# Kernel tuning notes

Measured on AMD Instinct MI355X. Metric: run time of the kernel, lower is better.

## Reference

```python
import jax, jax.numpy as jnp
import numpy as np

B, D, O = 16384, 1024, 2048
MU, LAM = 0.9, 0.1


def setup_inputs() -> dict:
    key = jax.random.key(0)
    ks = jax.random.split(key, 16)
    stdv = float(1.0 / np.sqrt(D))
    u = lambda k, shape, s: jax.random.uniform(k, shape, jnp.float32, -s, s)
    return {
        "x": jax.random.normal(ks[0], (B, D), jnp.float32),
        "x_ctx": jax.random.normal(ks[1], (B, D), jnp.float32),
        "classifier": u(ks[2], (O, D), stdv),
        "none_tensor": u(ks[3], (1, D), stdv),
        "ctx_q_w": u(ks[4], (O, D), stdv),
        "ctx_q_b": u(ks[5], (O,), stdv),
        "word_g_w": u(ks[6], (1, D), stdv),
        "word_g_b": u(ks[7], (1,), stdv),
        "tcq_w1": u(ks[8], (D, D), stdv),
        "tcq_b1": u(ks[9], (D,), stdv),
        "tcq_w2": u(ks[10], (O, D), stdv),
        "tcq_b2": u(ks[11], (O,), stdv),
        "history_input": 0.1 * jax.random.normal(ks[12], (O - 1, D), jnp.float32),
        "history_count": jax.random.randint(ks[13], (O - 1,), 0, 10),
        "labels": jax.random.randint(ks[14], (B,), 0, O),
    }


def reference(x, x_ctx, classifier, none_tensor, ctx_q_w, ctx_q_b,
              word_g_w, word_g_b, tcq_w1, tcq_b1, tcq_w2, tcq_b2,
              history_input, history_count, labels):
    mu, lam = MU, LAM
    # ---- update_history (torch.no_grad), vectorized over classes via segment_sum ----
    xs = jax.lax.stop_gradient(x)
    sums = jax.ops.segment_sum(xs, labels, num_segments=O)               # [O, D]
    counts = jax.ops.segment_sum(jnp.ones((B,), jnp.float32), labels, num_segments=O)  # [O]
    has = counts[1:] > 0                                                  # classes 1..O-1
    cls_mean = sums[1:] / jnp.maximum(counts[1:], 1.0)[:, None]
    hist = jnp.where(has[:, None], mu * history_input + cls_mean, history_input)
    cnt = history_count + has.astype(history_count.dtype)
    # ---- generate_substitute (mu < 1 branch) ----
    denom = 1.0 - jnp.power(mu, jnp.maximum(cnt, 1).astype(jnp.float32))[:, None]
    v = hist * (1.0 - mu) / denom                                        # [O-1, D]
    r_sub = jnp.concatenate([none_tensor, v], axis=0)                    # [O, D]
    ctx_logits = x_ctx @ ctx_q_w.T + ctx_q_b                              # [B, O]
    att_logits = jax.nn.gelu(x @ tcq_w1.T + tcq_b1, approximate=False) @ tcq_w2.T + tcq_b2  # [B, O]
    # ---- gated combine + bilinear classifier (training=True path: w uses ctx_logits) ----
    g_word = jax.nn.sigmoid(x @ word_g_w.T + word_g_b)                    # [B, 1]
    w = g_word * jax.nn.sigmoid(ctx_logits)                               # [B, O]
    # logits = sum(((1-w)*x[:,None,:] + w*r_sub) * classifier, -1), collapsed algebraically
    logits = (1.0 - w) * (x @ classifier.T) + w * jnp.einsum('od,od->o', r_sub, classifier)[None, :]
    # ---- losses on labels >= 0 (mask-weighted means, jit-safe) ----
    mask = (labels >= 0).astype(jnp.float32)
    n = jnp.maximum(mask.sum(), 1.0)
    lsm = jax.nn.log_softmax(logits, axis=-1)
    nll = -jnp.take_along_axis(lsm, jnp.maximum(labels, 0)[:, None], axis=1)[:, 0]
    ce = (mask * nll).sum() / n
    mse_row = jnp.mean((ctx_logits - att_logits) ** 2, axis=-1)
    mse = (mask * mse_row).sum() / n
    return (ce + lam * mse, logits)
```

## Files before the change

kernel.cpp:

```cpp
#include <hip/hip_runtime.h>
#include <cstdint>
#include <cstddef>

#define DEV __device__ __forceinline__

typedef __attribute__((ext_vector_type(4))) float f32x4;
typedef __attribute__((ext_vector_type(8))) short bf16x8;
typedef unsigned short ushort_t;
typedef __attribute__((ext_vector_type(8))) unsigned short ushort8;

static constexpr int B_ = 16384, D_ = 1024, O_ = 2048;
static constexpr float LAM_ = 0.1f;

static constexpr size_t WS_XBF   = 0;
static constexpr size_t WS_XCBF  = WS_XBF   + (size_t)B_ * D_ * 2;
static constexpr size_t WS_HBF   = WS_XCBF  + (size_t)B_ * D_ * 2;
static constexpr size_t WS_CLSBF = WS_HBF   + (size_t)B_ * D_ * 2;
static constexpr size_t WS_CTWBF = WS_CLSBF + (size_t)O_ * D_ * 2;
static constexpr size_t WS_W2BF  = WS_CTWBF + (size_t)O_ * D_ * 2;
static constexpr size_t WS_W1BF  = WS_W2BF  + (size_t)O_ * D_ * 2;
static constexpr size_t WS_SMALL = WS_W1BF  + (size_t)D_ * D_ * 2;
static constexpr size_t SM_COUNTS = 0;
static constexpr size_t SM_TSUM   = 8192;
static constexpr size_t SM_MSE    = 16384;
static constexpr size_t SM_ZERO_BYTES = 82176;
static constexpr size_t SM_S      = 82176;
static constexpr size_t SM_GWORD  = 90368;
static constexpr size_t SM_CEROW  = 155904;
static constexpr size_t SM_PMAX   = 262144;
static constexpr size_t SM_PSUM   = 262144 + 524288;
static constexpr size_t WS_CTXBF  = WS_SMALL + 2 * 1024 * 1024;
static constexpr size_t WS_NEED_BIG = WS_CTXBF + (size_t)B_ * O_ * 2;

DEV float wave_sum(float v) {
  #pragma unroll
  for (int o = 32; o; o >>= 1) v += __shfl_xor(v, o, 64);
  return v;
}

DEV ushort_t f2bf1(float f) {
  union { float f; unsigned u; } c{f};
  unsigned r = c.u + 0x7fffu + ((c.u >> 16) & 1u);
  return (ushort_t)(r >> 16);
}

DEV float bf2f(ushort_t u) {
  union { unsigned u; float f; } c{(unsigned)u << 16};
  return c.f;
}

DEV float sigmoidf(float z) { return 1.0f / (1.0f + expf(-z)); }

DEV void gload_lds16(const ushort_t* g, ushort_t* l) {
  __builtin_amdgcn_global_load_lds((const __attribute__((address_space(1))) void*)g,
                                   (__attribute__((address_space(3))) void*)l, 16, 0, 0);
}

DEV void stage2(const ushort_t* __restrict__ s0, ushort_t* slot, int tid) {
  gload_lds16(s0, slot + tid * 8);
  gload_lds16(s0 + 128 * 1024, slot + (tid + 512) * 8);
}

DEV void stage128s(const ushort_t* __restrict__ src, ushort_t* lds_, int tid) {
  int c0 = tid, c1 = tid + 256;
  int q0 = (c0 & 3) ^ ((c0 >> 3) & 3);
  int q1 = (c1 & 3) ^ ((c1 >> 3) & 3);
  gload_lds16(src + (size_t)(c0 >> 2) * 1024 + q0 * 8, lds_ + c0 * 8);
  gload_lds16(src + (size_t)(c1 >> 2) * 1024 + q1 * 8, lds_ + c1 * 8);
}

DEV f32x4 mfma16(bf16x8 a, bf16x8 b, f32x4 c) {
  return __builtin_amdgcn_mfma_f32_16x16x32_bf16(a, b, c, 0, 0, 0);
}

template<int N> DEV void wait_vm() {
  if constexpr (N == 8)      asm volatile("s_waitcnt vmcnt(8)" ::: "memory");
  else if constexpr (N == 4) asm volatile("s_waitcnt vmcnt(4)" ::: "memory");
  else if constexpr (N == 0) asm volatile("s_waitcnt vmcnt(0)" ::: "memory");
}

__global__ __launch_bounds__(256) void f2bf_kernel(const float* __restrict__ in,
                                                   ushort_t* __restrict__ out, int n8) {
  int i = blockIdx.x * 256 + threadIdx.x;
  if (i >= n8) return;
  const float4* p = (const float4*)(in + (size_t)i * 8);
  float4 a = p[0], b = p[1];
  ushort8 o;
  o[0] = f2bf1(a.x); o[1] = f2bf1(a.y); o[2] = f2bf1(a.z); o[3] = f2bf1(a.w);
  o[4] = f2bf1(b.x); o[5] = f2bf1(b.y); o[6] = f2bf1(b.z); o[7] = f2bf1(b.w);
  *(ushort8*)(out + (size_t)i * 8) = o;
}

__global__ __launch_bounds__(256) void rowdot_kernel(const float* __restrict__ x,
    const float* __restrict__ cls, const float* __restrict__ wg,
    const float* __restrict__ wgb, const int* __restrict__ labels,
    float* __restrict__ tsum, float* __restrict__ counts, float* __restrict__ g_word) {
  int wave = threadIdx.x >> 6, lane = threadIdx.x & 63;
  int row = blockIdx.x * 4 + wave;
  const float* xr = x + (size_t)row * D_;
  int lab = labels[row];
  const float* cr = cls + (size_t)max(lab, 0) * D_;
  float t = 0.f, g = 0.f;
  #pragma unroll
  for (int j = 0; j < 4; ++j) {
    int d = j * 256 + lane * 4;
    float4 xv = *(const float4*)(xr + d);
    float4 cv = *(const float4*)(cr + d);
    float4 wv = *(const float4*)(wg + d);
    t += xv.x * cv.x + xv.y * cv.y + xv.z * cv.z + xv.w * cv.w;
    g += xv.x * wv.x + xv.y * wv.y + xv.z * wv.z + xv.w * wv.w;
  }
  t = wave_sum(t); g = wave_sum(g);
  if (lane == 0) {
    if (lab >= 0) {
      atomicAdd(&tsum[lab], t);
      atomicAdd(&counts[lab], 1.0f);
    }
    g_word[row] = sigmoidf(g + wgb[0]);
  }
}

__global__ __launch_bounds__(256) void scls_kernel(const float* __restrict__ cls,
    const float* __restrict__ none_t, const float* __restrict__ hist,
    const int* __restrict__ hcnt, const float* __restrict__ counts,
    const float* __restrict__ tsum, float* __restrict__ s) {
  int wave = threadIdx.x >> 6, lane = threadIdx.x & 63;
  int o = blockIdx.x * 4 + wave;
  if (o >= O_) return;
  const float* cr = cls + (size_t)o * D_;
  const float* src = (o == 0) ? none_t : hist + (size_t)(o - 1) * D_;
  float dv = 0.f;
  #pragma unroll
  for (int j = 0; j < 4; ++j) {
    int d = j * 256 + lane * 4;
    float4 a = *(const float4*)(src + d);
    float4 c = *(const float4*)(cr + d);
    dv += a.x * c.x + a.y * c.y + a.z * c.z + a.w * c.w;
  }
  dv = wave_sum(dv);
  if (lane == 0) {
    if (o == 0) { s[0] = dv; }
    else {
      float co = counts[o];
      bool has = co > 0.f;
      int cnt = hcnt[o - 1] + (has ? 1 : 0);
      float denom = 1.f - powf(0.9f, (float)max(cnt, 1));
      float val = has ? (0.9f * dv + tsum[o] / fmaxf(co, 1.f)) : dv;
      s[o] = (0.1f / denom) * val;
    }
  }
}

template<bool S01, bool S23, int W1, int W3>
DEV void tile8(int t, const ushort_t* __restrict__ sA0, const ushort_t* __restrict__ sB0,
               ushort_t* lds, int tid, int aoff, int boff, f32x4 (&acc)[8][4]) {
  const int k0 = 2 * t, k1 = 2 * t + 1;
  const ushort_t* As0 = lds + (k0 & 3) * 8192;
  const ushort_t* Bs0 = lds + 32768 + (k0 & 3) * 8192;
  const ushort_t* As1 = lds + (k1 & 3) * 8192;
  const ushort_t* Bs1 = lds + 32768 + (k1 & 3) * 8192;
  bf16x8 afr[4], bfr[4];
  #pragma unroll
  for (int n = 0; n < 4; n++) bfr[n] = *(const bf16x8*)&Bs0[boff + n * 512];
  #pragma unroll
  for (int m = 0; m < 4; m++) afr[m] = *(const bf16x8*)&As0[aoff + m * 512];
  if constexpr (S01) stage2(sA0 + (size_t)(2 * t + 3) * 32, lds + ((2 * t + 3) & 3) * 8192, tid);
  __builtin_amdgcn_s_barrier();
  __builtin_amdgcn_s_setprio(1);
  #pragma unroll
  for (int m = 0; m < 4; m++)
    #pragma unroll
    for (int n = 0; n < 4; n++) acc[m][n] = mfma16(afr[m], bfr[n], acc[m][n]);
  __builtin_amdgcn_s_setprio(0);
  __builtin_amdgcn_s_barrier();
  #pragma unroll
  for (int m = 0; m < 4; m++) afr[m] = *(const bf16x8*)&As0[aoff + (m + 4) * 512];
  if constexpr (S01) stage2(sB0 + (size_t)(2 * t + 3) * 32, lds + 32768 + ((2 * t + 3) & 3) * 8192, tid);
  __builtin_amdgcn_s_barrier();
  __builtin_amdgcn_s_setprio(1);
  #pragma unroll
  for (int m = 0; m < 4; m++)
    #pragma unroll
    for (int n = 0; n < 4; n++) acc[m + 4][n] = mfma16(afr[m], bfr[n], acc[m + 4][n]);
  __builtin_amdgcn_s_setprio(0);
  wait_vm<W1>();
  __builtin_amdgcn_s_barrier();
  #pragma unroll
  for (int n = 0; n < 4; n++) bfr[n] = *(const bf16x8*)&Bs1[boff + n * 512];
  #pragma unroll
  for (int m = 0; m < 4; m++) afr[m] = *(const bf16x8*)&As1[aoff + m * 512];
  if constexpr (S23) stage2(sA0 + (size_t)(2 * t + 4) * 32, lds + ((2 * t + 4) & 3) * 8192, tid);
  __builtin_amdgcn_s_barrier();
  __builtin_amdgcn_s_setprio(1);
  #pragma unroll
  for (int m = 0; m < 4; m++)
    #pragma unroll
    for (int n = 0; n < 4; n++) acc[m][n] = mfma16(afr[m], bfr[n], acc[m][n]);
  __builtin_amdgcn_s_setprio(0);
  __builtin_amdgcn_s_barrier();
  #pragma unroll
  for (int m = 0; m < 4; m++) afr[m] = *(const bf16x8*)&As1[aoff + (m + 4) * 512];
  if constexpr (S23) stage2(sB0 + (size_t)(2 * t + 4) * 32, lds + 32768 + ((2 * t + 4) & 3) * 8192, tid);
  __builtin_amdgcn_s_barrier();
  __builtin_amdgcn_s_setprio(1);
  #pragma unroll
  for (int m = 0; m < 4; m++)
    #pragma unroll
    for (int n = 0; n < 4; n++) acc[m + 4][n] = mfma16(afr[m], bfr[n], acc[m + 4][n]);
  __builtin_amdgcn_s_setprio(0);
  wait_vm<W3>();
  __builtin_amdgcn_s_barrier();
}

template<int EPI, int NTSHIFT, bool CTXB>
__global__ __launch_bounds__(512, 2) void gemm8_kernel(
    const ushort_t* __restrict__ A, const ushort_t* __restrict__ Bmat,
    const float* __restrict__ bias, float* __restrict__ fout,
    ushort_t* __restrict__ hout, ushort_t* __restrict__ ctxbf,
    const float* __restrict__ g_word, const float* __restrict__ svec,
    float* __restrict__ pmax, float* __restrict__ psum) {
  __shared__ __align__(16) ushort_t lds[65536];
  const int tid = threadIdx.x, lane = tid & 63, wave = tid >> 6;
  const int wr = wave >> 2, wc = wave & 3;
  const int nwg = 64 << NTSHIFT, cpx = nwg >> 3;
  int bid = blockIdx.x;
  int wg = (bid & 7) * cpx + (bid >> 3);
  const int bm = wg >> NTSHIFT, bn = wg & ((1 << NTSHIFT) - 1);
  const int NCOL = 256 << NTSHIFT;
  const int qsrc = (tid & 3) ^ ((tid >> 3) & 3);
  const ushort_t* sA0 = A + ((size_t)bm * 256 + (tid >> 2)) * 1024 + qsrc * 8;
  const ushort_t* sB0 = Bmat + ((size_t)bn * 256 + (tid >> 2)) * 1024 + qsrc * 8;
  const int qrd = (lane >> 4) ^ (((lane & 15) >> 1) & 3);
  const int aoff = (wr * 128 + (lane & 15)) * 32 + qrd * 8;
  const int boff = (wc * 64 + (lane & 15)) * 32 + qrd * 8;
  f32x4 acc[8][4] = {};
  stage2(sA0, lds, tid);
  stage2(sB0, lds + 32768, tid);
  stage2(sA0 + 32, lds + 8192, tid);
  stage2(sB0 + 32, lds + 32768 + 8192, tid);
  stage2(sA0 + 64, lds + 2 * 8192, tid);
  stage2(sB0 + 64, lds + 32768 + 2 * 8192, tid);
  wait_vm<8>();
  __builtin_amdgcn_s_barrier();
  for (int t = 0; t < 14; ++t)
    tile8<true, true, 8, 8>(t, sA0, sB0, lds, tid, aoff, boff, acc);
  tile8<true, false, 8, 4>(14, sA0, sB0, lds, tid, aoff, boff, acc);
  tile8<false, false, 0, -1>(15, sA0, sB0, lds, tid, aoff, boff, acc);
  float* lred = (float*)lds;
  #pragma unroll
  for (int m = 0; m < 8; m++) {
    #pragma unroll
    for (int i = 0; i < 4; i++) {
      int rloc = wr * 128 + m * 16 + (lane >> 4) * 4 + i;
      int row = bm * 256 + rloc;
      if constexpr (EPI == 0 || EPI == 1) {
        #pragma unroll
        for (int n = 0; n < 4; n++) {
          int col = bn * 256 + wc * 64 + n * 16 + (lane & 15);
          float v = acc[m][n][i] + bias[col];
          if constexpr (EPI == 0) {
            float gl = 0.5f * v * (1.f + erff(v * 0.70710678118f));
            hout[(size_t)row * 1024 + col] = f2bf1(gl);
          } else if constexpr (CTXB) {
            ctxbf[(size_t)row * O_ + col] = f2bf1(v);
          } else {
            fout[(size_t)row * NCOL + col] = v;
          }
        }
      } else {
        float gw = g_word[row];
        float vals[4];
        float vmax = -INFINITY;
        #pragma unroll
        for (int n = 0; n < 4; n++) {
          int col = bn * 256 + wc * 64 + n * 16 + (lane & 15);
          size_t off = (size_t)row * NCOL + col;
          float ctx = CTXB ? bf2f(ctxbf[(size_t)row * O_ + col]) : fout[off];
          float w = gw * sigmoidf(ctx);
          float lv = (1.f - w) * acc[m][n][i] + w * svec[col];
          fout[off] = lv;
          vals[n] = lv;
          vmax = fmaxf(vmax, lv);
        }
        #pragma unroll
        for (int o = 1; o < 16; o <<= 1) vmax = fmaxf(vmax, __shfl_xor(vmax, o, 64));
        float se = 0.f;
        #pragma unroll
        for (int n = 0; n < 4; n++) se += expf(vals[n] - vmax);
        #pragma unroll
        for (int o = 1; o < 16; o <<= 1) se += __shfl_xor(se, o, 64);
        if ((lane & 15) == 0) {
          lred[(wc * 256 + rloc) * 2] = vmax;
          lred[(wc * 256 + rloc) * 2 + 1] = se;
        }
      }
    }
  }
  if constexpr (EPI == 3) {
    __syncthreads();
    if (tid < 256) {
      float M = -INFINITY;
      #pragma unroll
      for (int j = 0; j < 4; j++) M = fmaxf(M, lred[(j * 256 + tid) * 2]);
      float S = 0.f;
      #pragma unroll
      for (int j = 0; j < 4; j++)
        S += lred[(j * 256 + tid) * 2 + 1] * expf(lred[(j * 256 + tid) * 2] - M);
      size_t gi = (size_t)bn * B_ + bm * 256 + tid;
      pmax[gi] = M;
      psum[gi] = S;
    }
  }
}

template<bool CTXB>
__global__ __launch_bounds__(256, 3) void gemm128_att(
    const ushort_t* __restrict__ A, const ushort_t* __restrict__ Bmat,
    const float* __restrict__ bias, const float* __restrict__ fout,
    const ushort_t* __restrict__ ctxbf, float* __restrict__ mse_row) {
  __shared__ __align__(16) ushort_t As[128 * 32], Bs[128 * 32];
  const int tid = threadIdx.x, lane = tid & 63, wave = tid >> 6;
  const int wr = wave >> 1, wc = wave & 1;
  int bid = blockIdx.x;
  int group = bid >> 7, within = bid & 127;
  int bm = group * 8 + (within & 7);
  int bn = within >> 3;
  f32x4 acc[4][4] = {};
  const ushort_t* Ap = A + (size_t)bm * 128 * 1024;
  const ushort_t* Bp = Bmat + (size_t)bn * 128 * 1024;
  const int r = lane & 15;
  const int qrd8 = ((lane >> 4) ^ ((r >> 1) & 3)) * 8;
  for (int k0 = 0; k0 < 1024; k0 += 32) {
    stage128s(Ap + k0, As, tid);
    stage128s(Bp + k0, Bs, tid);
    asm volatile("s_waitcnt vmcnt(0)" ::: "memory");
    __builtin_amdgcn_s_barrier();
    bf16x8 af[4], bf[4];
    #pragma unroll
    for (int m = 0; m < 4; m++) af[m] = *(const bf16x8*)&As[(wr * 64 + m * 16 + r) * 32 + qrd8];
    #pragma unroll
    for (int n = 0; n < 4; n++) bf[n] = *(const bf16x8*)&Bs[(wc * 64 + n * 16 + r) * 32 + qrd8];
    #pragma unroll
    for (int m = 0; m < 4; m++)
      #pragma unroll
      for (int n = 0; n < 4; n++) acc[m][n] = mfma16(af[m], bf[n], acc[m][n]);
    __builtin_amdgcn_s_barrier();
  }
  #pragma unroll
  for (int m = 0; m < 4; m++) {
    #pragma unroll
    for (int i = 0; i < 4; i++) {
      int row = bm * 128 + wr * 64 + m * 16 + (lane >> 4) * 4 + i;
      float msum = 0.f;
      #pragma unroll
      for (int n = 0; n < 4; n++) {
        int col = bn * 128 + wc * 64 + n * 16 + (lane & 15);
        float att = acc[m][n][i] + bias[col];
        float ctx = CTXB ? bf2f(ctxbf[(size_t)row * O_ + col])
                         : fout[(size_t)row * O_ + col];
        float d = ctx - att;
        msum += d * d;
      }
      #pragma unroll
      for (int o = 1; o < 16; o <<= 1) msum += __shfl_xor(msum, o, 64);
      if ((lane & 15) == 0) atomicAdd(&mse_row[row], msum);
    }
  }
}

__global__ __launch_bounds__(256) void ce_fin_kernel(const float* __restrict__ logits,
    const float* __restrict__ pmax, const float* __restrict__ psum,
    const int* __restrict__ labels, float* __restrict__ ce_row) {
  int row = blockIdx.x * 256 + threadIdx.x;
  float M = -INFINITY;
  #pragma unroll
  for (int j = 0; j < 8; j++) M = fmaxf(M, pmax[(size_t)j * B_ + row]);
  float S = 0.f;
  #pragma unroll
  for (int j = 0; j < 8; j++)
    S += psum[(size_t)j * B_ + row] * expf(pmax[(size_t)j * B_ + row] - M);
  int lab = labels[row];
  float nll = 0.f;
  if (lab >= 0) nll = -(logits[(size_t)row * O_ + lab] - M - logf(S));
  ce_row[row] = nll;
}

__global__ __launch_bounds__(256) void finalize_kernel(const float* __restrict__ ce_row,
    const float* __restrict__ mse_row, const int* __restrict__ labels,
    float* __restrict__ out0) {
  int t = threadIdx.x, lane = t & 63, wave = t >> 6;
  float sn = 0.f, sm = 0.f, sc = 0.f;
  for (int i = t; i < B_; i += 256) {
    if (labels[i] >= 0) { sn += ce_row[i]; sm += mse_row[i]; sc += 1.f; }
  }
  sn = wave_sum(sn); sm = wave_sum(sm); sc = wave_sum(sc);
  __shared__ float r0[4], r1[4], r2[4];
  if (lane == 0) { r0[wave] = sn; r1[wave] = sm; r2[wave] = sc; }
  __syncthreads();
  if (t == 0) {
    float a = r0[0] + r0[1] + r0[2] + r0[3];
    float b = r1[0] + r1[1] + r1[2] + r1[3];
    float c = r2[0] + r2[1] + r2[2] + r2[3];
    out0[0] = (a + LAM_ * (b / (float)O_)) / fmaxf(c, 1.f);
  }
}

extern "C" void kernel_launch(void* const* d_in, const int* in_sizes, int n_in,
                              void* d_out, int out_size, void* d_ws, size_t ws_size,
                              hipStream_t stream) {
  const float* x        = (const float*)d_in[0];
  const float* x_ctx    = (const float*)d_in[1];
  const float* cls      = (const float*)d_in[2];
  const float* none_t   = (const float*)d_in[3];
  const float* ctx_q_w  = (const float*)d_in[4];
  const float* ctx_q_b  = (const float*)d_in[5];
  const float* word_g_w = (const float*)d_in[6];
  const float* word_g_b = (const float*)d_in[7];
  const float* w1       = (const float*)d_in[8];
  const float* b1       = (const float*)d_in[9];
  const float* w2       = (const float*)d_in[10];
  const float* b2       = (const float*)d_in[11];
  const float* hist     = (const float*)d_in[12];
  const int*   hcnt     = (const int*)d_in[13];
  const int*   labels   = (const int*)d_in[14];

  float* out  = (float*)d_out;
  float* out1 = out + 1;
  char* ws = (char*)d_ws;

  ushort_t* xbf   = (ushort_t*)(ws + WS_XBF);
  ushort_t* xcbf  = (ushort_t*)(ws + WS_XCBF);
  ushort_t* hbf   = (ushort_t*)(ws + WS_HBF);
  ushort_t* clsbf = (ushort_t*)(ws + WS_CLSBF);
  ushort_t* ctwbf = (ushort_t*)(ws + WS_CTWBF);
  ushort_t* w2bf  = (ushort_t*)(ws + WS_W2BF);
  ushort_t* w1bf  = (ushort_t*)(ws + WS_W1BF);
  float* counts   = (float*)(ws + WS_SMALL + SM_COUNTS);
  float* tsum     = (float*)(ws + WS_SMALL + SM_TSUM);
  float* mse_row  = (float*)(ws + WS_SMALL + SM_MSE);
  float* s        = (float*)(ws + WS_SMALL + SM_S);
  float* g_word   = (float*)(ws + WS_SMALL + SM_GWORD);
  float* ce_row   = (float*)(ws + WS_SMALL + SM_CEROW);
  float* pmax     = (float*)(ws + WS_SMALL + SM_PMAX);
  float* psum     = (float*)(ws + WS_SMALL + SM_PSUM);
  ushort_t* ctxbf = (ushort_t*)(ws + WS_CTXBF);
  const bool big  = ws_size >= WS_NEED_BIG;

  hipMemsetAsync(ws + WS_SMALL, 0, SM_ZERO_BYTES, stream);

  f2bf_kernel<<<8192, 256, 0, stream>>>(x, xbf, B_ * D_ / 8);
  f2bf_kernel<<<8192, 256, 0, stream>>>(x_ctx, xcbf, B_ * D_ / 8);
  f2bf_kernel<<<1024, 256, 0, stream>>>(cls, clsbf, O_ * D_ / 8);
  f2bf_kernel<<<1024, 256, 0, stream>>>(ctx_q_w, ctwbf, O_ * D_ / 8);
  f2bf_kernel<<<1024, 256, 0, stream>>>(w2, w2bf, O_ * D_ / 8);
  f2bf_kernel<<<512, 256, 0, stream>>>(w1, w1bf, D_ * D_ / 8);

  rowdot_kernel<<<B_ / 4, 256, 0, stream>>>(x, cls, word_g_w, word_g_b, labels,
                                            tsum, counts, g_word);
  scls_kernel<<<O_ / 4, 256, 0, stream>>>(cls, none_t, hist, hcnt, counts, tsum, s);

  gemm8_kernel<0, 2, false><<<256, 512, 0, stream>>>(xbf, w1bf, b1, nullptr, hbf,
                                                     nullptr, nullptr, nullptr,
                                                     nullptr, nullptr);
  if (big)
    gemm8_kernel<1, 3, true><<<512, 512, 0, stream>>>(xcbf, ctwbf, ctx_q_b, out1,
                                                      nullptr, ctxbf, nullptr, nullptr,
                                                      nullptr, nullptr);
  else
    gemm8_kernel<1, 3, false><<<512, 512, 0, stream>>>(xcbf, ctwbf, ctx_q_b, out1,
                                                       nullptr, nullptr, nullptr, nullptr,
                                                       nullptr, nullptr);
  if (big)
    gemm128_att<true><<<2048, 256, 0, stream>>>(hbf, w2bf, b2, out1, ctxbf, mse_row);
  else
    gemm128_att<false><<<2048, 256, 0, stream>>>(hbf, w2bf, b2, out1, nullptr, mse_row);
  if (big)
    gemm8_kernel<3, 3, true><<<512, 512, 0, stream>>>(xbf, clsbf, nullptr, out1,
                                                      nullptr, ctxbf, g_word, s,
                                                      pmax, psum);
  else
    gemm8_kernel<3, 3, false><<<512, 512, 0, stream>>>(xbf, clsbf, nullptr, out1,
                                                       nullptr, nullptr, g_word, s,
                                                       pmax, psum);

  ce_fin_kernel<<<B_ / 256, 256, 0, stream>>>(out1, pmax, psum, labels, ce_row);
  finalize_kernel<<<1, 256, 0, stream>>>(ce_row, mse_row, labels, out);
}
```

Measured before the change: 460.5 us.

## Fuse x bf16 conversion into rowdot and move softmax stats to separate CE pass

The fp32-to-bf16 conversion of x now happens inside the row-dot kernel, which already reads x, so one full pass over x is removed. The per-tile log-softmax partial max/sum reduction is dropped from the classifier GEMM epilogue. Instead a new per-row CE kernel rereads the full logits (128 MB) and computes max and logsumexp itself. This lightens the GEMM epilogue and removes its LDS reduction and syncthreads, at the cost of an extra full read of the logits.

```diff
diff --git a/kernel.cpp b/kernel.cpp
--- a/kernel.cpp
+++ b/kernel.cpp
@@ -27,8 +27,6 @@
 static constexpr size_t SM_S      = 82176;
 static constexpr size_t SM_GWORD  = 90368;
 static constexpr size_t SM_CEROW  = 155904;
-static constexpr size_t SM_PMAX   = 262144;
-static constexpr size_t SM_PSUM   = 262144 + 524288;
 static constexpr size_t WS_CTXBF  = WS_SMALL + 2 * 1024 * 1024;
 static constexpr size_t WS_NEED_BIG = WS_CTXBF + (size_t)B_ * O_ * 2;
 
@@ -91,9 +89,10 @@
   *(ushort8*)(out + (size_t)i * 8) = o;
 }
 
-__global__ __launch_bounds__(256) void rowdot_kernel(const float* __restrict__ x,
+__global__ __launch_bounds__(256) void rowdot_cvt_kernel(const float* __restrict__ x,
     const float* __restrict__ cls, const float* __restrict__ wg,
     const float* __restrict__ wgb, const int* __restrict__ labels,
+    ushort_t* __restrict__ xbf,
     float* __restrict__ tsum, float* __restrict__ counts, float* __restrict__ g_word) {
   int wave = threadIdx.x >> 6, lane = threadIdx.x & 63;
   int row = blockIdx.x * 4 + wave;
@@ -109,6 +108,10 @@
     float4 wv = *(const float4*)(wg + d);
     t += xv.x * cv.x + xv.y * cv.y + xv.z * cv.z + xv.w * cv.w;
     g += xv.x * wv.x + xv.y * wv.y + xv.z * wv.z + xv.w * wv.w;
+    uint2 pk;
+    pk.x = (unsigned)f2bf1(xv.x) | ((unsigned)f2bf1(xv.y) << 16);
+    pk.y = (unsigned)f2bf1(xv.z) | ((unsigned)f2bf1(xv.w) << 16);
+    *(uint2*)(xbf + (size_t)row * D_ + d) = pk;
   }
   t = wave_sum(t); g = wave_sum(g);
   if (lane == 0) {
@@ -217,8 +220,7 @@
     const ushort_t* __restrict__ A, const ushort_t* __restrict__ Bmat,
     const float* __restrict__ bias, float* __restrict__ fout,
     ushort_t* __restrict__ hout, ushort_t* __restrict__ ctxbf,
-    const float* __restrict__ g_word, const float* __restrict__ svec,
-    float* __restrict__ pmax, float* __restrict__ psum) {
+    const float* __restrict__ g_word, const float* __restrict__ svec) {
   __shared__ __align__(16) ushort_t lds[65536];
   const int tid = threadIdx.x, lane = tid & 63, wave = tid >> 6;
   const int wr = wave >> 2, wc = wave & 3;
@@ -246,69 +248,32 @@
     tile8<true, true, 8, 8>(t, sA0, sB0, lds, tid, aoff, boff, acc);
   tile8<true, false, 8, 4>(14, sA0, sB0, lds, tid, aoff, boff, acc);
   tile8<false, false, 0, -1>(15, sA0, sB0, lds, tid, aoff, boff, acc);
-  float* lred = (float*)lds;
   #pragma unroll
   for (int m = 0; m < 8; m++) {
     #pragma unroll
     for (int i = 0; i < 4; i++) {
-      int rloc = wr * 128 + m * 16 + (lane >> 4) * 4 + i;
-      int row = bm * 256 + rloc;
-      if constexpr (EPI == 0 || EPI == 1) {
-        #pragma unroll
-        for (int n = 0; n < 4; n++) {
-          int col = bn * 256 + wc * 64 + n * 16 + (lane & 15);
-          float v = acc[m][n][i] + bias[col];
-          if constexpr (EPI == 0) {
-            float gl = 0.5f * v * (1.f + erff(v * 0.70710678118f));
-            hout[(size_t)row * 1024 + col] = f2bf1(gl);
-          } else if constexpr (CTXB) {
-            ctxbf[(size_t)row * O_ + col] = f2bf1(v);
-          } else {
-            fout[(size_t)row * NCOL + col] = v;
-          }
-        }
-      } else {
-        float gw = g_word[row];
-        float vals[4];
-        float vmax = -INFINITY;
-        #pragma unroll
-        for (int n = 0; n < 4; n++) {
-          int col = bn * 256 + wc * 64 + n * 16 + (lane & 15);
+      int row = bm * 256 + wr * 128 + m * 16 + (lane >> 4) * 4 + i;
+      float gw = 0.f;
+      if constexpr (EPI == 3) gw = g_word[row];
+      #pragma unroll
+      for (int n = 0; n < 4; n++) {
+        int col = bn * 256 + wc * 64 + n * 16 + (lane & 15);
+        float v = acc[m][n][i];
+        if constexpr (EPI == 0) {
+          float z = v + bias[col];
+          float gl = 0.5f * z * (1.f + erff(z * 0.70710678118f));
+          hout[(size_t)row * 1024 + col] = f2bf1(gl);
+        } else if constexpr (EPI == 1) {
+          float z = v + bias[col];
+          if constexpr (CTXB) ctxbf[(size_t)row * O_ + col] = f2bf1(z);
+          else                fout[(size_t)row * NCOL + col] = z;
+        } else {
           size_t off = (size_t)row * NCOL + col;
           float ctx = CTXB ? bf2f(ctxbf[(size_t)row * O_ + col]) : fout[off];
           float w = gw * sigmoidf(ctx);
-          float lv = (1.f - w) * acc[m][n][i] + w * svec[col];
-          fout[off] = lv;
-          vals[n] = lv;
-          vmax = fmaxf(vmax, lv);
-        }
-        #pragma unroll
-        for (int o = 1; o < 16; o <<= 1) vmax = fmaxf(vmax, __shfl_xor(vmax, o, 64));
-        float se = 0.f;
-        #pragma unroll
-        for (int n = 0; n < 4; n++) se += expf(vals[n] - vmax);
-        #pragma unroll
-        for (int o = 1; o < 16; o <<= 1) se += __shfl_xor(se, o, 64);
-        if ((lane & 15) == 0) {
-          lred[(wc * 256 + rloc) * 2] = vmax;
-          lred[(wc * 256 + rloc) * 2 + 1] = se;
+          fout[off] = (1.f - w) * v + w * svec[col];
         }
       }
-    }
-  }
-  if constexpr (EPI == 3) {
-    __syncthreads();
-    if (tid < 256) {
-      float M = -INFINITY;
-      #pragma unroll
-      for (int j = 0; j < 4; j++) M = fmaxf(M, lred[(j * 256 + tid) * 2]);
-      float S = 0.f;
-      #pragma unroll
-      for (int j = 0; j < 4; j++)
-        S += lred[(j * 256 + tid) * 2 + 1] * expf(lred[(j * 256 + tid) * 2] - M);
-      size_t gi = (size_t)bn * B_ + bm * 256 + tid;
-      pmax[gi] = M;
-      psum[gi] = S;
     }
   }
 }
@@ -368,21 +333,33 @@
   }
 }
 
-__global__ __launch_bounds__(256) void ce_fin_kernel(const float* __restrict__ logits,
-    const float* __restrict__ pmax, const float* __restrict__ psum,
+__global__ __launch_bounds__(256) void ce_kernel(const float* __restrict__ logits,
     const int* __restrict__ labels, float* __restrict__ ce_row) {
-  int row = blockIdx.x * 256 + threadIdx.x;
-  float M = -INFINITY;
-  #pragma unroll
-  for (int j = 0; j < 8; j++) M = fmaxf(M, pmax[(size_t)j * B_ + row]);
-  float S = 0.f;
-  #pragma unroll
-  for (int j = 0; j < 8; j++)
-    S += psum[(size_t)j * B_ + row] * expf(pmax[(size_t)j * B_ + row] - M);
-  int lab = labels[row];
-  float nll = 0.f;
-  if (lab >= 0) nll = -(logits[(size_t)row * O_ + lab] - M - logf(S));
-  ce_row[row] = nll;
+  int row = blockIdx.x, t = threadIdx.x, lane = t & 63, wave = t >> 6;
+  const float* lr = logits + (size_t)row * O_;
+  float v[8];
+  float m = -INFINITY;
+  #pragma unroll
+  for (int j = 0; j < 8; j++) { v[j] = lr[t + j * 256]; m = fmaxf(m, v[j]); }
+  #pragma unroll
+  for (int o = 32; o; o >>= 1) m = fmaxf(m, __shfl_xor(m, o, 64));
+  __shared__ float red[8];
+  if (lane == 0) red[wave] = m;
+  __syncthreads();
+  m = fmaxf(fmaxf(red[0], red[1]), fmaxf(red[2], red[3]));
+  float se = 0.f;
+  #pragma unroll
+  for (int j = 0; j < 8; j++) se += expf(v[j] - m);
+  se = wave_sum(se);
+  if (lane == 0) red[4 + wave] = se;
+  __syncthreads();
+  if (t == 0) {
+    float bs = red[4] + red[5] + red[6] + red[7];
+    int lab = labels[row];
+    float nll = 0.f;
+    if (lab >= 0) nll = -(lr[lab] - m - logf(bs));
+    ce_row[row] = nll;
+  }
 }
 
 __global__ __launch_bounds__(256) void finalize_kernel(const float* __restrict__ ce_row,
@@ -441,48 +418,40 @@
   float* s        = (float*)(ws + WS_SMALL + SM_S);
   float* g_word   = (float*)(ws + WS_SMALL + SM_GWORD);
   float* ce_row   = (float*)(ws + WS_SMALL + SM_CEROW);
-  float* pmax     = (float*)(ws + WS_SMALL + SM_PMAX);
-  float* psum     = (float*)(ws + WS_SMALL + SM_PSUM);
   ushort_t* ctxbf = (ushort_t*)(ws + WS_CTXBF);
   const bool big  = ws_size >= WS_NEED_BIG;
 
   hipMemsetAsync(ws + WS_SMALL, 0, SM_ZERO_BYTES, stream);
 
-  f2bf_kernel<<<8192, 256, 0, stream>>>(x, xbf, B_ * D_ / 8);
+  rowdot_cvt_kernel<<<B_ / 4, 256, 0, stream>>>(x, cls, word_g_w, word_g_b, labels,
+                                                xbf, tsum, counts, g_word);
   f2bf_kernel<<<8192, 256, 0, stream>>>(x_ctx, xcbf, B_ * D_ / 8);
   f2bf_kernel<<<1024, 256, 0, stream>>>(cls, clsbf, O_ * D_ / 8);
   f2bf_kernel<<<1024, 256, 0, stream>>>(ctx_q_w, ctwbf, O_ * D_ / 8);
   f2bf_kernel<<<1024, 256, 0, stream>>>(w2, w2bf, O_ * D_ / 8);
   f2bf_kernel<<<512, 256, 0, stream>>>(w1, w1bf, D_ * D_ / 8);
 
-  rowdot_kernel<<<B_ / 4, 256, 0, stream>>>(x, cls, word_g_w, word_g_b, labels,
-                                            tsum, counts, g_word);
   scls_kernel<<<O_ / 4, 256, 0, stream>>>(cls, none_t, hist, hcnt, counts, tsum, s);
 
   gemm8_kernel<0, 2, false><<<256, 512, 0, stream>>>(xbf, w1bf, b1, nullptr, hbf,
-                                                     nullptr, nullptr, nullptr,
-                                                     nullptr, nullptr);
+                                                     nullptr, nullptr, nullptr);
   if (big)
     gemm8_kernel<1, 3, true><<<512, 512, 0, stream>>>(xcbf, ctwbf, ctx_q_b, out1,
-                                                      nullptr, ctxbf, nullptr, nullptr,
-                                                      nullptr, nullptr);
+                                                      nullptr, ctxbf, nullptr, nullptr);
   else
     gemm8_kernel<1, 3, false><<<512, 512, 0, stream>>>(xcbf, ctwbf, ctx_q_b, out1,
-                                                       nullptr, nullptr, nullptr, nullptr,
-                                                       nullptr, nullptr);
+                                                       nullptr, nullptr, nullptr, nullptr);
   if (big)
     gemm128_att<true><<<2048, 256, 0, stream>>>(hbf, w2bf, b2, out1, ctxbf, mse_row);
   else
     gemm128_att<false><<<2048, 256, 0, stream>>>(hbf, w2bf, b2, out1, nullptr, mse_row);
   if (big)
     gemm8_kernel<3, 3, true><<<512, 512, 0, stream>>>(xbf, clsbf, nullptr, out1,
-                                                      nullptr, ctxbf, g_word, s,
-                                                      pmax, psum);
+                                                      nullptr, ctxbf, g_word, s);
   else
     gemm8_kernel<3, 3, false><<<512, 512, 0, stream>>>(xbf, clsbf, nullptr, out1,
-                                                       nullptr, nullptr, g_word, s,
-                                                       pmax, psum);
-
-  ce_fin_kernel<<<B_ / 256, 256, 0, stream>>>(out1, pmax, psum, labels, ce_row);
+                                                       nullptr, nullptr, g_word, s);
+
+  ce_kernel<<<B_, 256, 0, stream>>>(out1, labels, ce_row);
   finalize_kernel<<<1, 256, 0, stream>>>(ce_row, mse_row, labels, out);
 }
```

Measured after the change: 434.3 us. 1.06x faster.
